# Kernel tuning notes

Hardware: AMD Instinct MI355X
Metric: run time of the kernel (lower is better)

The kernel has to match this reference:

```python
import jax, jax.numpy as jnp
import numpy as np

NNODES = 128
BS = 1024
MAX_ST = (NNODES + 1) ** 2   # 16641
MAX_ST1 = NNODES ** 2        # 16384
AT_LEN = NNODES + 1          # 129
MAXOUT = AT_LEN + MAX_ST + MAX_ST1  # 33154
HIDDEN = 512
OUT_DIM = AT_LEN             # 129


def setup_inputs() -> dict:
    key = jax.random.key(0)
    ks = jax.random.split(key, 6)
    st = jax.random.normal(ks[0], (BS, MAX_ST), dtype=jnp.float32)
    at = jax.random.normal(ks[1], (BS, AT_LEN), dtype=jnp.float32)
    st1 = jax.random.normal(ks[2], (BS, MAX_ST1), dtype=jnp.float32)
    # MLP params (self.layers): Linear(MAXOUT->HIDDEN) + ReLU + Linear(HIDDEN->OUT_DIM)
    W1 = jax.random.normal(ks[3], (MAXOUT, HIDDEN), dtype=jnp.float32) * (1.0 / np.sqrt(MAXOUT))
    b1 = jnp.zeros((HIDDEN,), dtype=jnp.float32)
    W2 = jax.random.normal(ks[4], (HIDDEN, OUT_DIM), dtype=jnp.float32) * (1.0 / np.sqrt(HIDDEN))
    b2 = jnp.zeros((OUT_DIM,), dtype=jnp.float32)
    return {"st": st, "at": at, "st1": st1, "W1": W1, "b1": b1, "W2": W2, "b2": b2}


def reference(st, at, st1, W1, b1, W2, b2):
    # Batched equivalent of the per-sample Python loop:
    # per sample: cat(pad(st.flatten(), maxSt), at, pad(st1.flatten(), maxSt1)) -> layers -> cat outputs.
    # st/st1 are already at padded sizes here, so concat directly along features.
    x = jnp.concatenate([st, at, st1], axis=1)          # [B, MAXOUT]
    h = jax.nn.relu(x @ W1 + b1)                        # [B, HIDDEN]
    out = h @ W2 + b2                                   # [B, OUT_DIM]
    return out.reshape(-1)                              # concatenated 1-D outputs, matching torch.cat
```

## Files before the change

kernel.cpp:

```cpp
#include <hip/hip_runtime.h>

#define BATCH 1024
#define STSZ 16641
#define ATSZ 129
#define ST1SZ 16384
#define K1 33154
#define K1P 33280
#define HID 512
#define ODIM 129
#define NKT 520
#define NSLICE 32

typedef __bf16 bf16;
typedef bf16 bf16x8 __attribute__((ext_vector_type(8)));
typedef float floatx4 __attribute__((ext_vector_type(4)));
typedef float f32x4u __attribute__((ext_vector_type(4), aligned(4)));

typedef __attribute__((address_space(3))) unsigned int as3_uint;
typedef __attribute__((address_space(1))) unsigned int as1_uint;

__device__ __forceinline__ unsigned short f2bf(float f) {
  unsigned int u = __float_as_uint(f);
  unsigned int r = (u + 0x7FFFu + ((u >> 16) & 1u)) >> 16;
  return (unsigned short)r;
}
__device__ __forceinline__ float bf2f(unsigned short s) {
  unsigned int u = ((unsigned int)s) << 16;
  return __uint_as_float(u);
}

__device__ __forceinline__ void gload_lds16(const unsigned short* g, unsigned short* l) {
  __builtin_amdgcn_global_load_lds((const as1_uint*)g, (as3_uint*)l, 16, 0, 0);
}

__global__ __launch_bounds__(256) void packX(const float* __restrict__ st,
                                             const float* __restrict__ at,
                                             const float* __restrict__ st1,
                                             unsigned short* __restrict__ Xb) {
  int b = blockIdx.y;
  int g = blockIdx.x * 256 + threadIdx.x;
  if (g >= K1P / 4) return;
  int col = g * 4;
  const float* srow  = st  + (long)b * STSZ;
  const float* arow  = at  + (long)b * ATSZ;
  const float* s1row = st1 + (long)b * ST1SZ;

  float4 v;
  if (col + 3 < STSZ) {
    f32x4u t = *(const f32x4u*)(srow + col);
    v = make_float4(t.x, t.y, t.z, t.w);
  } else if (col >= STSZ + ATSZ && col + 3 < K1) {
    f32x4u t = *(const f32x4u*)(s1row + (col - (STSZ + ATSZ)));
    v = make_float4(t.x, t.y, t.z, t.w);
  } else if (col >= STSZ && col + 3 < STSZ + ATSZ) {
    f32x4u t = *(const f32x4u*)(arow + (col - STSZ));
    v = make_float4(t.x, t.y, t.z, t.w);
  } else if (col >= K1) {
    v = make_float4(0.f, 0.f, 0.f, 0.f);
  } else {
    float e[4];
#pragma unroll
    for (int j = 0; j < 4; ++j) {
      int p = col + j;
      if (p < STSZ)                 e[j] = srow[p];
      else if (p < STSZ + ATSZ)     e[j] = arow[p - STSZ];
      else if (p < K1)              e[j] = s1row[p - (STSZ + ATSZ)];
      else                          e[j] = 0.f;
    }
    v = make_float4(e[0], e[1], e[2], e[3]);
  }
  unsigned short o[4] = { f2bf(v.x), f2bf(v.y), f2bf(v.z), f2bf(v.w) };
  *(ushort4*)&Xb[(long)b * K1P + col] = *(const ushort4*)o;
}

__global__ __launch_bounds__(256) void packW1(const float* __restrict__ W1,
                                              unsigned short* __restrict__ W1t) {
  __shared__ unsigned short tile[64][72];
  int k0 = blockIdx.x * 64;
  int n0 = blockIdx.y * 64;
  int tid = threadIdx.x;
  int nt = (tid & 15) * 4;
  int kr = tid >> 4;
#pragma unroll
  for (int p = 0; p < 4; ++p) {
    int k = p * 16 + kr;
    int kk = k0 + k;
    float4 v = make_float4(0.f, 0.f, 0.f, 0.f);
    if (kk < K1) v = *(const float4*)&W1[(long)kk * HID + n0 + nt];
    unsigned short o[4] = { f2bf(v.x), f2bf(v.y), f2bf(v.z), f2bf(v.w) };
    *(ushort4*)&tile[k][nt] = *(const ushort4*)o;
  }
  __syncthreads();
  int kt = (tid & 15) * 4;
  int nr = tid >> 4;
#pragma unroll
  for (int p = 0; p < 4; ++p) {
    int n = p * 16 + nr;
    unsigned short o[4] = { tile[kt][n], tile[kt + 1][n], tile[kt + 2][n], tile[kt + 3][n] };
    *(ushort4*)&W1t[(long)(n0 + n) * K1P + k0 + kt] = *(const ushort4*)o;
  }
}

__global__ __launch_bounds__(256, 2) void gemm1(const unsigned short* __restrict__ Xb,
                                                const unsigned short* __restrict__ W1t,
                                                unsigned short* __restrict__ part) {
  __shared__ __align__(16) unsigned short lA[128 * 64];
  __shared__ __align__(16) unsigned short lB[128 * 64];

  int nt = blockIdx.x;
  int mt = blockIdx.y;
  int s  = blockIdx.z;
  int t0 = s * 16 + (s < 8 ? s : 8);
  int tc = 16 + (s < 8 ? 1 : 0);

  int tid = threadIdx.x;
  int wave = tid >> 6;
  int lane = tid & 63;
  int wm = (wave & 1) * 64;
  int wn = (wave >> 1) * 64;

  floatx4 acc[4][4] = {};

  const unsigned short* Ab = Xb  + (long)(mt * 128) * K1P;
  const unsigned short* Bb = W1t + (long)(nt * 128) * K1P;

  int srow = lane >> 3;
  int scol = ((lane & 7) ^ srow) * 8;

  int sr = lane & 7;

  for (int it = 0; it < tc; ++it) {
    long kOff = (long)(t0 + it) * 64;
#pragma unroll
    for (int r = 0; r < 4; ++r) {
      int c = wave * 4 + r;
      int row = c * 8 + srow;
      gload_lds16(Ab + (long)row * K1P + kOff + scol, &lA[c * 512 + lane * 8]);
      gload_lds16(Bb + (long)row * K1P + kOff + scol, &lB[c * 512 + lane * 8]);
    }
    __syncthreads();
#pragma unroll
    for (int ks = 0; ks < 2; ++ks) {
      int q = ks * 4 + (lane >> 4);
      int kidx = ((q ^ sr)) * 8;
      bf16x8 af[4], bfr[4];
#pragma unroll
      for (int i = 0; i < 4; ++i)
        af[i] = *(const bf16x8*)&lA[(wm + i * 16 + (lane & 15)) * 64 + kidx];
#pragma unroll
      for (int j = 0; j < 4; ++j)
        bfr[j] = *(const bf16x8*)&lB[(wn + j * 16 + (lane & 15)) * 64 + kidx];
#pragma unroll
      for (int i = 0; i < 4; ++i)
#pragma unroll
        for (int j = 0; j < 4; ++j)
          acc[i][j] = __builtin_amdgcn_mfma_f32_16x16x32_bf16(af[i], bfr[j], acc[i][j], 0, 0, 0);
    }
    __syncthreads();
  }

  unsigned short* P = part + (long)s * BATCH * HID;
  int cn = nt * 128 + wn + (lane & 15);
  int rbase = mt * 128 + wm + (lane >> 4) * 4;
#pragma unroll
  for (int i = 0; i < 4; ++i)
#pragma unroll
    for (int j = 0; j < 4; ++j)
#pragma unroll
      for (int r = 0; r < 4; ++r)
        P[(long)(rbase + i * 16 + r) * HID + cn + j * 16] = f2bf(acc[i][j][r]);
}

__global__ __launch_bounds__(256) void reduceBias(const unsigned short* __restrict__ part,
                                                  const float* __restrict__ b1,
                                                  float* __restrict__ h) {
  int e4 = blockIdx.x * 256 + threadIdx.x;
  float4 a = ((const float4*)b1)[e4 & (HID / 4 - 1)];
#pragma unroll
  for (int s = 0; s < NSLICE; ++s) {
    ushort4 p = ((const ushort4*)part)[(long)s * (BATCH * HID / 4) + e4];
    a.x += bf2f(p.x); a.y += bf2f(p.y); a.z += bf2f(p.z); a.w += bf2f(p.w);
  }
  a.x = fmaxf(a.x, 0.f); a.y = fmaxf(a.y, 0.f);
  a.z = fmaxf(a.z, 0.f); a.w = fmaxf(a.w, 0.f);
  ((float4*)h)[e4] = a;
}

__global__ __launch_bounds__(256) void gemm2(const float* __restrict__ h,
                                             const float* __restrict__ W2,
                                             const float* __restrict__ b2,
                                             float* __restrict__ out) {
  __shared__ float hs[HID];
  int m = blockIdx.x;
  int t = threadIdx.x;
#pragma unroll
  for (int i = t; i < HID; i += 256) hs[i] = h[(long)m * HID + i];
  __syncthreads();
  if (t < ODIM) {
    float a = b2[t];
#pragma unroll 8
    for (int k = 0; k < HID; ++k) a += hs[k] * W2[k * ODIM + t];
    out[(long)m * ODIM + t] = a;
  }
}

extern "C" void kernel_launch(void* const* d_in, const int* in_sizes, int n_in,
                              void* d_out, int out_size, void* d_ws, size_t ws_size,
                              hipStream_t stream) {
  const float* st  = (const float*)d_in[0];
  const float* at  = (const float*)d_in[1];
  const float* st1 = (const float*)d_in[2];
  const float* W1  = (const float*)d_in[3];
  const float* b1  = (const float*)d_in[4];
  const float* W2  = (const float*)d_in[5];
  const float* b2  = (const float*)d_in[6];
  float* out = (float*)d_out;

  char* ws = (char*)d_ws;
  unsigned short* Xb   = (unsigned short*)ws;
  unsigned short* W1t  = (unsigned short*)(ws + (size_t)BATCH * K1P * 2);
  unsigned short* part = (unsigned short*)(ws + (size_t)BATCH * K1P * 2 + (size_t)HID * K1P * 2);
  float* h = (float*)(ws + (size_t)BATCH * K1P * 2 + (size_t)HID * K1P * 2
                      + (size_t)NSLICE * BATCH * HID * 2);

  packX<<<dim3((K1P / 4 + 255) / 256, BATCH), 256, 0, stream>>>(st, at, st1, Xb);
  packW1<<<dim3(NKT, HID / 64), 256, 0, stream>>>(W1, W1t);
  gemm1<<<dim3(4, 8, NSLICE), 256, 0, stream>>>(Xb, W1t, part);
  reduceBias<<<dim3(BATCH * HID / 4 / 256), 256, 0, stream>>>(part, b1, h);
  gemm2<<<dim3(BATCH), 256, 0, stream>>>(h, W2, b2, out);
}
```

Measured before the change: 326.8 us.

## Load GEMM1 fragments directly from global into registers with double buffering

```diff
diff --git a/kernel.cpp b/kernel.cpp
--- a/kernel.cpp
+++ b/kernel.cpp
@@ -16,9 +16,6 @@
 typedef float floatx4 __attribute__((ext_vector_type(4)));
 typedef float f32x4u __attribute__((ext_vector_type(4), aligned(4)));
 
-typedef __attribute__((address_space(3))) unsigned int as3_uint;
-typedef __attribute__((address_space(1))) unsigned int as1_uint;
-
 __device__ __forceinline__ unsigned short f2bf(float f) {
   unsigned int u = __float_as_uint(f);
   unsigned int r = (u + 0x7FFFu + ((u >> 16) & 1u)) >> 16;
@@ -27,10 +24,6 @@
 __device__ __forceinline__ float bf2f(unsigned short s) {
   unsigned int u = ((unsigned int)s) << 16;
   return __uint_as_float(u);
-}
-
-__device__ __forceinline__ void gload_lds16(const unsigned short* g, unsigned short* l) {
-  __builtin_amdgcn_global_load_lds((const as1_uint*)g, (as3_uint*)l, 16, 0, 0);
 }
 
 __global__ __launch_bounds__(256) void packX(const float* __restrict__ st,
@@ -104,9 +97,6 @@
 __global__ __launch_bounds__(256, 2) void gemm1(const unsigned short* __restrict__ Xb,
                                                 const unsigned short* __restrict__ W1t,
                                                 unsigned short* __restrict__ part) {
-  __shared__ __align__(16) unsigned short lA[128 * 64];
-  __shared__ __align__(16) unsigned short lB[128 * 64];
-
   int nt = blockIdx.x;
   int mt = blockIdx.y;
   int s  = blockIdx.z;
@@ -118,49 +108,59 @@
   int lane = tid & 63;
   int wm = (wave & 1) * 64;
   int wn = (wave >> 1) * 64;
+  int m15 = lane & 15;
+  int kl = (lane >> 4) * 8;
 
   floatx4 acc[4][4] = {};
 
-  const unsigned short* Ab = Xb  + (long)(mt * 128) * K1P;
-  const unsigned short* Bb = W1t + (long)(nt * 128) * K1P;
-
-  int srow = lane >> 3;
-  int scol = ((lane & 7) ^ srow) * 8;
-
-  int sr = lane & 7;
-
+  const char* Ap = (const char*)Xb;
+  const char* Bp = (const char*)W1t;
+
+  unsigned int aOff[4], bOff[4];
+#pragma unroll
+  for (int i = 0; i < 4; ++i)
+    aOff[i] = ((unsigned int)(mt * 128 + wm + i * 16 + m15) * K1P + (unsigned int)(t0 * 64 + kl)) * 2u;
+#pragma unroll
+  for (int j = 0; j < 4; ++j)
+    bOff[j] = ((unsigned int)(nt * 128 + wn + j * 16 + m15) * K1P + (unsigned int)(t0 * 64 + kl)) * 2u;
+
+  bf16x8 Af[2][2][4], Bf[2][2][4];
+
+#pragma unroll
+  for (int i = 0; i < 4; ++i) {
+    Af[0][0][i] = *(const bf16x8*)(Ap + aOff[i]);
+    Af[0][1][i] = *(const bf16x8*)(Ap + aOff[i] + 64);
+    Bf[0][0][i] = *(const bf16x8*)(Bp + bOff[i]);
+    Bf[0][1][i] = *(const bf16x8*)(Bp + bOff[i] + 64);
+  }
+#pragma unroll
+  for (int i = 0; i < 4; ++i) { aOff[i] += 128; bOff[i] += 128; }
+
+#pragma unroll 2
   for (int it = 0; it < tc; ++it) {
-    long kOff = (long)(t0 + it) * 64;
-#pragma unroll
-    for (int r = 0; r < 4; ++r) {
-      int c = wave * 4 + r;
-      int row = c * 8 + srow;
-      gload_lds16(Ab + (long)row * K1P + kOff + scol, &lA[c * 512 + lane * 8]);
-      gload_lds16(Bb + (long)row * K1P + kOff + scol, &lB[c * 512 + lane * 8]);
+    int cur = it & 1, nxt = cur ^ 1;
+    if (it + 1 < tc) {
+#pragma unroll
+      for (int i = 0; i < 4; ++i) {
+        Af[nxt][0][i] = *(const bf16x8*)(Ap + aOff[i]);
+        Af[nxt][1][i] = *(const bf16x8*)(Ap + aOff[i] + 64);
+        Bf[nxt][0][i] = *(const bf16x8*)(Bp + bOff[i]);
+        Bf[nxt][1][i] = *(const bf16x8*)(Bp + bOff[i] + 64);
+      }
+#pragma unroll
+      for (int i = 0; i < 4; ++i) { aOff[i] += 128; bOff[i] += 128; }
     }
-    __syncthreads();
-#pragma unroll
-    for (int ks = 0; ks < 2; ++ks) {
-      int q = ks * 4 + (lane >> 4);
-      int kidx = ((q ^ sr)) * 8;
-      bf16x8 af[4], bfr[4];
+#pragma unroll
+    for (int ks = 0; ks < 2; ++ks)
 #pragma unroll
       for (int i = 0; i < 4; ++i)
-        af[i] = *(const bf16x8*)&lA[(wm + i * 16 + (lane & 15)) * 64 + kidx];
-#pragma unroll
-      for (int j = 0; j < 4; ++j)
-        bfr[j] = *(const bf16x8*)&lB[(wn + j * 16 + (lane & 15)) * 64 + kidx];
-#pragma unroll
-      for (int i = 0; i < 4; ++i)
 #pragma unroll
         for (int j = 0; j < 4; ++j)
-          acc[i][j] = __builtin_amdgcn_mfma_f32_16x16x32_bf16(af[i], bfr[j], acc[i][j], 0, 0, 0);
-    }
-    __syncthreads();
+          acc[i][j] = __builtin_amdgcn_mfma_f32_16x16x32_bf16(Af[cur][ks][i], Bf[cur][ks][j], acc[i][j], 0, 0, 0);
   }
 
   unsigned short* P = part + (long)s * BATCH * HID;
-  int cn = nt * 128 + wn + (lane & 15);
+  int cn = nt * 128 + wn + m15;
   int rbase = mt * 128 + wm + (lane >> 4) * 4;
 #pragma unroll
   for (int i = 0; i < 4; ++i)
```

New measurement: 737.9 us. 2.26x slower.
